# Performance work log

Measured on AMD Instinct MI355X. Metric: run time of the kernel, lower is better.

## Reference

```python
import jax, jax.numpy as jnp
import numpy as np

OFFSET = 1
NUM_ENTITY = 128

def setup_inputs() -> dict:
    key = jax.random.key(0)
    ks = jax.random.split(key, 8)
    B, L, D = 32, 2048, 1024
    M, E, S = 256, NUM_ENTITY, 128
    H, P = 2048, 512
    return {
        "sequence_output": jax.random.normal(ks[0], (B, L, D), dtype=jnp.float32),
        "mention_pos": jax.random.randint(ks[1], (B, M), 0, L - 2),
        "mention2entity": jnp.sort(jax.random.randint(ks[2], (B, M), 0, E), axis=-1),
        "sent_pos": jax.random.randint(ks[3], (B, S), 0, L - 2),
        "fc1_w": jax.random.normal(ks[4], (D, H), dtype=jnp.float32) * 0.02,
        "fc1_b": jnp.zeros((H,), dtype=jnp.float32),
        "fc2_w": jax.random.normal(ks[5], (H, P), dtype=jnp.float32) * 0.02,
        "fc2_b": jnp.zeros((P,), dtype=jnp.float32),
    }

def _segment_logsumexp(x, seg):
    # x: [M, D] mention embeddings, seg: [M] entity ids -> [E, D]
    m = jax.ops.segment_max(x, seg, num_segments=NUM_ENTITY)           # [E, D]
    m_safe = jnp.where(jnp.isfinite(m), m, 0.0)
    s = jax.ops.segment_sum(jnp.exp(x - m_safe[seg]), seg, num_segments=NUM_ENTITY)
    cnt = jax.ops.segment_sum(jnp.ones((x.shape[0],), x.dtype), seg, num_segments=NUM_ENTITY)
    s_safe = jnp.where(cnt[:, None] > 0, s, 1.0)
    lse = jnp.log(s_safe) + m_safe
    # entities with no mentions stay zero (torch.zeros init in original)
    return jnp.where(cnt[:, None] > 0, lse, 0.0)

def reference(sequence_output, mention_pos, mention2entity, sent_pos, fc1_w, fc1_b, fc2_w, fc2_b):
    # gather mention start-token states (offset = +1 as in self.offset)
    mention_embed = jnp.take_along_axis(
        sequence_output, (mention_pos + OFFSET)[:, :, None], axis=1)  # [B, M, D]
    sent_embed = jnp.take_along_axis(
        sequence_output, (sent_pos + OFFSET)[:, :, None], axis=1)     # [B, S, D]
    entity_embed = jax.vmap(_segment_logsumexp)(mention_embed, mention2entity)  # [B, E, D]
    nodes = jnp.concatenate([mention_embed, entity_embed, sent_embed], axis=1)  # [B, M+E+S, D]
    # projection(): fc1 then fc2 (no nonlinearity, as in the original)
    h = jnp.einsum('bnd,dh->bnh', nodes, fc1_w) + fc1_b
    return jnp.einsum('bnh,hp->bnp', h, fc2_w) + fc2_b
```

## Files before the change

### kernel.cpp

```cpp
#include <hip/hip_runtime.h>
#include <cstdint>

#define DEV __device__ __forceinline__

typedef __attribute__((ext_vector_type(8))) short short8;
typedef __attribute__((ext_vector_type(4))) float f32x4;

DEV unsigned short f2bf(float f) {
    uint32_t u = __builtin_bit_cast(uint32_t, f);
    u += 0x7fffu + ((u >> 16) & 1u);
    return (unsigned short)(u >> 16);
}

DEV uint2 pack4(float4 v) {
    uint2 o;
    o.x = (uint32_t)f2bf(v.x) | ((uint32_t)f2bf(v.y) << 16);
    o.y = (uint32_t)f2bf(v.z) | ((uint32_t)f2bf(v.w) << 16);
    return o;
}

DEV void async_copy16(void* lds, const void* g) {
    __builtin_amdgcn_global_load_lds(
        (const __attribute__((address_space(1))) void*)g,
        (__attribute__((address_space(3))) void*)lds, 16, 0, 0);
}

template <int KLEN, int KSTR, int N>
DEV void gemm_body_part(const unsigned short* __restrict__ A,
                        const unsigned short* __restrict__ Bt,
                        float* __restrict__ P,
                        int Mtot, int rowblk, int colblk, int zidx,
                        unsigned short* Al, unsigned short* Bl) {
    int t = threadIdx.x;
    int lane = t & 63, w = t >> 6;
    int wm = w >> 1, wn = w & 1;
    int row0 = rowblk * 128, col0 = colblk * 128;
    size_t kbase = (size_t)zidx * KLEN;
    f32x4 acc[4][4] = {};

    int rifc = lane >> 2;
    int koff = (lane & 3) * 8;
    int c0 = 2 * w, c1 = 2 * w + 1;

    const unsigned short* Abase = A + (size_t)row0 * KSTR + kbase + koff;
    const unsigned short* Bbase = Bt + (size_t)col0 * KSTR + kbase + koff;

    for (int kt = 0; kt < KLEN / 32; ++kt) {
        int k0 = kt * 32;
        __syncthreads();
        async_copy16(&Al[c0 * 512], Abase + (size_t)(c0 * 16 + rifc) * KSTR + k0);
        async_copy16(&Al[c1 * 512], Abase + (size_t)(c1 * 16 + rifc) * KSTR + k0);
        async_copy16(&Bl[c0 * 512], Bbase + (size_t)(c0 * 16 + rifc) * KSTR + k0);
        async_copy16(&Bl[c1 * 512], Bbase + (size_t)(c1 * 16 + rifc) * KSTR + k0);
        __syncthreads();

        int r = lane & 15, kq = lane >> 4;
        short8 a[4], b[4];
        #pragma unroll
        for (int mi = 0; mi < 4; ++mi)
            a[mi] = *reinterpret_cast<const short8*>(&Al[(wm * 64 + mi * 16 + r) * 32 + kq * 8]);
        #pragma unroll
        for (int ni = 0; ni < 4; ++ni)
            b[ni] = *reinterpret_cast<const short8*>(&Bl[(wn * 64 + ni * 16 + r) * 32 + kq * 8]);
        #pragma unroll
        for (int mi = 0; mi < 4; ++mi)
            #pragma unroll
            for (int ni = 0; ni < 4; ++ni)
                acc[mi][ni] = __builtin_amdgcn_mfma_f32_16x16x32_bf16(a[mi], b[ni], acc[mi][ni], 0, 0, 0);
    }

    int r = lane & 15, kq = lane >> 4;
    float* Pz = P + (size_t)zidx * (size_t)N * (size_t)Mtot;
    #pragma unroll
    for (int mi = 0; mi < 4; ++mi)
        #pragma unroll
        for (int ni = 0; ni < 4; ++ni) {
            int col = col0 + wn * 64 + ni * 16 + r;
            #pragma unroll
            for (int j = 0; j < 4; ++j) {
                int row = row0 + wm * 64 + mi * 16 + kq * 4 + j;
                Pz[(size_t)col * Mtot + row] = acc[mi][ni][j];
            }
        }
}

__global__ __launch_bounds__(256) void k_prep(const float* __restrict__ W1,
                                              const float* __restrict__ W2,
                                              const float* __restrict__ b1,
                                              unsigned short* __restrict__ W1c,
                                              unsigned short* __restrict__ W2t,
                                              float* __restrict__ part) {
    __shared__ unsigned short sh[32][33];
    int blk = blockIdx.x, t = threadIdx.x;
    if (blk < 2048) {
        int i = blk * 256 + t;
        float4 v = reinterpret_cast<const float4*>(W1)[i];
        reinterpret_cast<uint2*>(W1c)[i] = pack4(v);
    } else if (blk < 3072) {
        int idx = blk - 2048;
        int h0 = (idx & 63) * 32, p0 = (idx >> 6) * 32;
        int r = t >> 3, c4 = (t & 7) * 4;
        float4 v = *reinterpret_cast<const float4*>(&W2[(size_t)(h0 + r) * 512 + p0 + c4]);
        sh[r][c4 + 0] = f2bf(v.x);
        sh[r][c4 + 1] = f2bf(v.y);
        sh[r][c4 + 2] = f2bf(v.z);
        sh[r][c4 + 3] = f2bf(v.w);
        __syncthreads();
        uint2 o;
        o.x = (uint32_t)sh[c4 + 0][r] | ((uint32_t)sh[c4 + 1][r] << 16);
        o.y = (uint32_t)sh[c4 + 2][r] | ((uint32_t)sh[c4 + 3][r] << 16);
        *reinterpret_cast<uint2*>(&W2t[(size_t)(p0 + r) * 2048 + h0 + c4]) = o;
    } else {
        int hs = blk - 3072;
        float a0 = 0.f, a1 = 0.f;
        #pragma unroll 4
        for (int hh = 0; hh < 32; ++hh) {
            int h = hs * 32 + hh;
            float bb = b1[h];
            a0 += bb * W2[(size_t)h * 512 + t];
            a1 += bb * W2[(size_t)h * 512 + 256 + t];
        }
        part[hs * 512 + t] = a0;
        part[hs * 512 + 256 + t] = a1;
    }
}

__global__ __launch_bounds__(256) void k_mid(const float* __restrict__ seq,
                                             const int* __restrict__ mpos,
                                             const int* __restrict__ m2e,
                                             const unsigned short* __restrict__ W1c,
                                             const unsigned short* __restrict__ W2t,
                                             float* __restrict__ Wpart,
                                             const float* __restrict__ part,
                                             const float* __restrict__ b2,
                                             float* __restrict__ fb,
                                             unsigned short* __restrict__ ent) {
    __shared__ unsigned short Al[128 * 32];
    __shared__ unsigned short Bl[128 * 32];
    __shared__ int sm[256];
    __shared__ int sp[256];
    __shared__ int slo, shi;
    int blk = blockIdx.x, t = threadIdx.x;
    if (blk < 128) {
        gemm_body_part<512, 2048, 512>(W1c, W2t, Wpart, 1024,
                                       (blk >> 2) & 7, blk & 3, blk >> 5, Al, Bl);
    } else if (blk < 130) {
        int p = (blk - 128) * 256 + t;
        float s = b2[p];
        #pragma unroll
        for (int hs = 0; hs < 64; ++hs) s += part[hs * 512 + p];
        fb[p] = s;
    } else {
        int idx = blk - 130;
        int b = idx >> 7, e = idx & 127;
        sm[t] = m2e[b * 256 + t];
        sp[t] = mpos[b * 256 + t] + 1;
        if (t == 0) { slo = 0; shi = 0; }
        __syncthreads();
        if (sm[t] == e && (t == 0 || sm[t - 1] != e)) slo = t;
        if (sm[t] == e && (t == 255 || sm[t + 1] != e)) shi = t + 1;
        __syncthreads();
        int lo = slo, hi = shi;
        float ox, oy, oz, ow;
        if (hi > lo) {
            float s0 = 0.f, s1 = 0.f, s2 = 0.f, s3 = 0.f;
            for (int j = lo; j < hi; ++j) {
                float4 v = *reinterpret_cast<const float4*>(
                    &seq[((size_t)b * 2048 + sp[j]) * 1024 + t * 4]);
                s0 += __expf(v.x); s1 += __expf(v.y);
                s2 += __expf(v.z); s3 += __expf(v.w);
            }
            ox = __logf(s0); oy = __logf(s1);
            oz = __logf(s2); ow = __logf(s3);
        } else {
            ox = oy = oz = ow = 0.f;
        }
        float4 o; o.x = ox; o.y = oy; o.z = oz; o.w = ow;
        *reinterpret_cast<uint2*>(&ent[((size_t)b * 128 + e) * 1024 + t * 4]) = pack4(o);
    }
}

__global__ __launch_bounds__(256) void k_wreduce(const float* __restrict__ P,
                                                 unsigned short* __restrict__ Wt) {
    const size_t SPLIT = 512u * 1024u;
    int i = blockIdx.x * 256 + threadIdx.x;
    float4 a = reinterpret_cast<const float4*>(P)[i];
    float4 b = reinterpret_cast<const float4*>(P + SPLIT)[i];
    float4 c = reinterpret_cast<const float4*>(P + 2 * SPLIT)[i];
    float4 d = reinterpret_cast<const float4*>(P + 3 * SPLIT)[i];
    float4 s;
    s.x = a.x + b.x + c.x + d.x;
    s.y = a.y + b.y + c.y + d.y;
    s.z = a.z + b.z + c.z + d.z;
    s.w = a.w + b.w + c.w + d.w;
    reinterpret_cast<uint2*>(Wt)[i] = pack4(s);
}

__global__ __launch_bounds__(256) void k_gemm_main(const float* __restrict__ seq,
                                                   const int* __restrict__ mpos,
                                                   const int* __restrict__ spos,
                                                   const unsigned short* __restrict__ ent,
                                                   const unsigned short* __restrict__ Wt,
                                                   float* __restrict__ C,
                                                   const float* __restrict__ fb) {
    __shared__ unsigned short Al[128 * 32];
    __shared__ unsigned short Bl[128 * 32];
    int p = blockIdx.x;
    int cpx = gridDim.x >> 3;
    int L = (p & 7) * cpx + (p >> 3);
    int colblk = L & 3;
    int rowblk = L >> 2;

    int t = threadIdx.x;
    int lane = t & 63, w = t >> 6;
    int wm = w >> 1, wn = w & 1;
    int row0 = rowblk * 128, col0 = colblk * 128;
    int b = rowblk >> 2, quad = rowblk & 3;
    f32x4 acc[4][4] = {};

    int rifc = lane >> 2;
    int koff = (lane & 3) * 8;
    int c0 = 2 * w, c1 = 2 * w + 1;
    const unsigned short* Bbase = Wt + (size_t)col0 * 1024 + koff;

    if (quad == 2) {
        const unsigned short* Abase = ent + (size_t)b * 128 * 1024 + koff;
        for (int kt = 0; kt < 32; ++kt) {
            int k0 = kt * 32;
            __syncthreads();
            async_copy16(&Al[c0 * 512], Abase + (size_t)(c0 * 16 + rifc) * 1024 + k0);
            async_copy16(&Al[c1 * 512], Abase + (size_t)(c1 * 16 + rifc) * 1024 + k0);
            async_copy16(&Bl[c0 * 512], Bbase + (size_t)(c0 * 16 + rifc) * 1024 + k0);
            async_copy16(&Bl[c1 * 512], Bbase + (size_t)(c1 * 16 + rifc) * 1024 + k0);
            __syncthreads();
            int r = lane & 15, kq = lane >> 4;
            short8 a[4], bf[4];
            #pragma unroll
            for (int mi = 0; mi < 4; ++mi)
                a[mi] = *reinterpret_cast<const short8*>(&Al[(wm * 64 + mi * 16 + r) * 32 + kq * 8]);
            #pragma unroll
            for (int ni = 0; ni < 4; ++ni)
                bf[ni] = *reinterpret_cast<const short8*>(&Bl[(wn * 64 + ni * 16 + r) * 32 + kq * 8]);
            #pragma unroll
            for (int mi = 0; mi < 4; ++mi)
                #pragma unroll
                for (int ni = 0; ni < 4; ++ni)
                    acc[mi][ni] = __builtin_amdgcn_mfma_f32_16x16x32_bf16(a[mi], bf[ni], acc[mi][ni], 0, 0, 0);
        }
    } else {
        int rloc = t >> 3;
        int cof = (t & 7) * 4;
        const float* rp0; const float* rp1; const float* rp2; const float* rp3;
        {
            int m0, m1, m2, m3;
            if (quad == 3) {
                m0 = spos[b * 128 + rloc] + 1;
                m1 = spos[b * 128 + 32 + rloc] + 1;
                m2 = spos[b * 128 + 64 + rloc] + 1;
                m3 = spos[b * 128 + 96 + rloc] + 1;
            } else {
                int mb = b * 256 + quad * 128;
                m0 = mpos[mb + rloc] + 1;
                m1 = mpos[mb + 32 + rloc] + 1;
                m2 = mpos[mb + 64 + rloc] + 1;
                m3 = mpos[mb + 96 + rloc] + 1;
            }
            rp0 = seq + ((size_t)b * 2048 + m0) * 1024 + cof;
            rp1 = seq + ((size_t)b * 2048 + m1) * 1024 + cof;
            rp2 = seq + ((size_t)b * 2048 + m2) * 1024 + cof;
            rp3 = seq + ((size_t)b * 2048 + m3) * 1024 + cof;
        }
        for (int kt = 0; kt < 32; ++kt) {
            int k0 = kt * 32;
            __syncthreads();
            async_copy16(&Bl[c0 * 512], Bbase + (size_t)(c0 * 16 + rifc) * 1024 + k0);
            async_copy16(&Bl[c1 * 512], Bbase + (size_t)(c1 * 16 + rifc) * 1024 + k0);
            float4 v0 = *reinterpret_cast<const float4*>(rp0 + k0);
            float4 v1 = *reinterpret_cast<const float4*>(rp1 + k0);
            float4 v2 = *reinterpret_cast<const float4*>(rp2 + k0);
            float4 v3 = *reinterpret_cast<const float4*>(rp3 + k0);
            *reinterpret_cast<uint2*>(&Al[(rloc) * 32 + cof])      = pack4(v0);
            *reinterpret_cast<uint2*>(&Al[(32 + rloc) * 32 + cof]) = pack4(v1);
            *reinterpret_cast<uint2*>(&Al[(64 + rloc) * 32 + cof]) = pack4(v2);
            *reinterpret_cast<uint2*>(&Al[(96 + rloc) * 32 + cof]) = pack4(v3);
            __syncthreads();
            int r = lane & 15, kq = lane >> 4;
            short8 a[4], bf[4];
            #pragma unroll
            for (int mi = 0; mi < 4; ++mi)
                a[mi] = *reinterpret_cast<const short8*>(&Al[(wm * 64 + mi * 16 + r) * 32 + kq * 8]);
            #pragma unroll
            for (int ni = 0; ni < 4; ++ni)
                bf[ni] = *reinterpret_cast<const short8*>(&Bl[(wn * 64 + ni * 16 + r) * 32 + kq * 8]);
            #pragma unroll
            for (int mi = 0; mi < 4; ++mi)
                #pragma unroll
                for (int ni = 0; ni < 4; ++ni)
                    acc[mi][ni] = __builtin_amdgcn_mfma_f32_16x16x32_bf16(a[mi], bf[ni], acc[mi][ni], 0, 0, 0);
        }
    }

    int r = lane & 15, kq = lane >> 4;
    #pragma unroll
    for (int mi = 0; mi < 4; ++mi)
        #pragma unroll
        for (int ni = 0; ni < 4; ++ni) {
            int col = col0 + wn * 64 + ni * 16 + r;
            float bv = fb[col];
            #pragma unroll
            for (int j = 0; j < 4; ++j) {
                int row = row0 + wm * 64 + mi * 16 + kq * 4 + j;
                C[(size_t)row * 512 + col] = acc[mi][ni][j] + bv;
            }
        }
}


extern "C" void kernel_launch(void* const* d_in, const int* in_sizes, int n_in,
                              void* d_out, int out_size, void* d_ws, size_t ws_size,
                              hipStream_t stream) {
    const float* seq  = (const float*)d_in[0];
    const int*   mpos = (const int*)d_in[1];
    const int*   m2e  = (const int*)d_in[2];
    const int*   spos = (const int*)d_in[3];
    const float* W1   = (const float*)d_in[4];
    const float* b1   = (const float*)d_in[5];
    const float* W2   = (const float*)d_in[6];
    const float* b2   = (const float*)d_in[7];
    float* out = (float*)d_out;

    char* ws = (char*)d_ws;
    unsigned short* W1c   = (unsigned short*)(ws);
    unsigned short* W2t   = (unsigned short*)(ws + (4u << 20));
    unsigned short* Wt    = (unsigned short*)(ws + (6u << 20));
    float*          Wpart = (float*)(ws + (8u << 20));
    float*          part  = (float*)(ws + (16u << 20));
    float*          fb    = (float*)(ws + (16u << 20) + (1u << 18));
    unsigned short* ent   = (unsigned short*)(ws + (24u << 20));

    k_prep<<<3136, 256, 0, stream>>>(W1, W2, b1, W1c, W2t, part);
    k_mid<<<4226, 256, 0, stream>>>(seq, mpos, m2e, W1c, W2t, Wpart, part, b2, fb, ent);
    k_wreduce<<<512, 256, 0, stream>>>(Wpart, Wt);
    k_gemm_main<<<512, 256, 0, stream>>>(seq, mpos, spos, ent, Wt, out, fb);
}
```

Measured before the change: 66.73 us.

## Fuse weight prep into mid kernel and double-buffer main GEMM

Removes the separate k_prep kernel. The W1·W2 split-K GEMM blocks now load fp32 weights directly, convert them to bf16 in LDS, and transpose W2 on the fly. The fused bias b1·W2 is folded into those blocks and accumulated with atomicAdd into a zeroed fb buffer, and b2 is added in the final GEMM epilogue. The main GEMM also gains double-buffered LDS with prefetch of the next K tile, so loads overlap the MFMA work. The trade-offs are an extra memset launch, atomics, and scattered 2-byte LDS stores for the transposed B tile.

```diff
diff --git a/kernel.cpp b/kernel.cpp
--- a/kernel.cpp
+++ b/kernel.cpp
@@ -25,114 +25,18 @@
         (__attribute__((address_space(3))) void*)lds, 16, 0, 0);
 }
 
-template <int KLEN, int KSTR, int N>
-DEV void gemm_body_part(const unsigned short* __restrict__ A,
-                        const unsigned short* __restrict__ Bt,
-                        float* __restrict__ P,
-                        int Mtot, int rowblk, int colblk, int zidx,
-                        unsigned short* Al, unsigned short* Bl) {
-    int t = threadIdx.x;
-    int lane = t & 63, w = t >> 6;
-    int wm = w >> 1, wn = w & 1;
-    int row0 = rowblk * 128, col0 = colblk * 128;
-    size_t kbase = (size_t)zidx * KLEN;
-    f32x4 acc[4][4] = {};
-
-    int rifc = lane >> 2;
-    int koff = (lane & 3) * 8;
-    int c0 = 2 * w, c1 = 2 * w + 1;
-
-    const unsigned short* Abase = A + (size_t)row0 * KSTR + kbase + koff;
-    const unsigned short* Bbase = Bt + (size_t)col0 * KSTR + kbase + koff;
-
-    for (int kt = 0; kt < KLEN / 32; ++kt) {
-        int k0 = kt * 32;
-        __syncthreads();
-        async_copy16(&Al[c0 * 512], Abase + (size_t)(c0 * 16 + rifc) * KSTR + k0);
-        async_copy16(&Al[c1 * 512], Abase + (size_t)(c1 * 16 + rifc) * KSTR + k0);
-        async_copy16(&Bl[c0 * 512], Bbase + (size_t)(c0 * 16 + rifc) * KSTR + k0);
-        async_copy16(&Bl[c1 * 512], Bbase + (size_t)(c1 * 16 + rifc) * KSTR + k0);
-        __syncthreads();
-
-        int r = lane & 15, kq = lane >> 4;
-        short8 a[4], b[4];
-        #pragma unroll
-        for (int mi = 0; mi < 4; ++mi)
-            a[mi] = *reinterpret_cast<const short8*>(&Al[(wm * 64 + mi * 16 + r) * 32 + kq * 8]);
-        #pragma unroll
-        for (int ni = 0; ni < 4; ++ni)
-            b[ni] = *reinterpret_cast<const short8*>(&Bl[(wn * 64 + ni * 16 + r) * 32 + kq * 8]);
-        #pragma unroll
-        for (int mi = 0; mi < 4; ++mi)
-            #pragma unroll
-            for (int ni = 0; ni < 4; ++ni)
-                acc[mi][ni] = __builtin_amdgcn_mfma_f32_16x16x32_bf16(a[mi], b[ni], acc[mi][ni], 0, 0, 0);
-    }
-
-    int r = lane & 15, kq = lane >> 4;
-    float* Pz = P + (size_t)zidx * (size_t)N * (size_t)Mtot;
-    #pragma unroll
-    for (int mi = 0; mi < 4; ++mi)
-        #pragma unroll
-        for (int ni = 0; ni < 4; ++ni) {
-            int col = col0 + wn * 64 + ni * 16 + r;
-            #pragma unroll
-            for (int j = 0; j < 4; ++j) {
-                int row = row0 + wm * 64 + mi * 16 + kq * 4 + j;
-                Pz[(size_t)col * Mtot + row] = acc[mi][ni][j];
-            }
-        }
-}
-
-__global__ __launch_bounds__(256) void k_prep(const float* __restrict__ W1,
-                                              const float* __restrict__ W2,
-                                              const float* __restrict__ b1,
-                                              unsigned short* __restrict__ W1c,
-                                              unsigned short* __restrict__ W2t,
-                                              float* __restrict__ part) {
-    __shared__ unsigned short sh[32][33];
-    int blk = blockIdx.x, t = threadIdx.x;
-    if (blk < 2048) {
-        int i = blk * 256 + t;
-        float4 v = reinterpret_cast<const float4*>(W1)[i];
-        reinterpret_cast<uint2*>(W1c)[i] = pack4(v);
-    } else if (blk < 3072) {
-        int idx = blk - 2048;
-        int h0 = (idx & 63) * 32, p0 = (idx >> 6) * 32;
-        int r = t >> 3, c4 = (t & 7) * 4;
-        float4 v = *reinterpret_cast<const float4*>(&W2[(size_t)(h0 + r) * 512 + p0 + c4]);
-        sh[r][c4 + 0] = f2bf(v.x);
-        sh[r][c4 + 1] = f2bf(v.y);
-        sh[r][c4 + 2] = f2bf(v.z);
-        sh[r][c4 + 3] = f2bf(v.w);
-        __syncthreads();
-        uint2 o;
-        o.x = (uint32_t)sh[c4 + 0][r] | ((uint32_t)sh[c4 + 1][r] << 16);
-        o.y = (uint32_t)sh[c4 + 2][r] | ((uint32_t)sh[c4 + 3][r] << 16);
-        *reinterpret_cast<uint2*>(&W2t[(size_t)(p0 + r) * 2048 + h0 + c4]) = o;
-    } else {
-        int hs = blk - 3072;
-        float a0 = 0.f, a1 = 0.f;
-        #pragma unroll 4
-        for (int hh = 0; hh < 32; ++hh) {
-            int h = hs * 32 + hh;
-            float bb = b1[h];
-            a0 += bb * W2[(size_t)h * 512 + t];
-            a1 += bb * W2[(size_t)h * 512 + 256 + t];
-        }
-        part[hs * 512 + t] = a0;
-        part[hs * 512 + 256 + t] = a1;
-    }
+DEV float bf2f(unsigned short s) {
+    uint32_t u = (uint32_t)s << 16;
+    return __builtin_bit_cast(float, u);
 }
 
 __global__ __launch_bounds__(256) void k_mid(const float* __restrict__ seq,
                                              const int* __restrict__ mpos,
                                              const int* __restrict__ m2e,
-                                             const unsigned short* __restrict__ W1c,
-                                             const unsigned short* __restrict__ W2t,
+                                             const float* __restrict__ W1,
+                                             const float* __restrict__ W2,
+                                             const float* __restrict__ b1,
                                              float* __restrict__ Wpart,
-                                             const float* __restrict__ part,
-                                             const float* __restrict__ b2,
                                              float* __restrict__ fb,
                                              unsigned short* __restrict__ ent) {
     __shared__ unsigned short Al[128 * 32];
@@ -142,16 +46,80 @@
     __shared__ int slo, shi;
     int blk = blockIdx.x, t = threadIdx.x;
     if (blk < 128) {
-        gemm_body_part<512, 2048, 512>(W1c, W2t, Wpart, 1024,
-                                       (blk >> 2) & 7, blk & 3, blk >> 5, Al, Bl);
-    } else if (blk < 130) {
-        int p = (blk - 128) * 256 + t;
-        float s = b2[p];
-        #pragma unroll
-        for (int hs = 0; hs < 64; ++hs) s += part[hs * 512 + p];
-        fb[p] = s;
+        int rowblk = (blk >> 2) & 7, colblk = blk & 3, z = blk >> 5;
+        int row0 = rowblk * 128, col0 = colblk * 128;
+        int kbase = z * 512;
+        int lane = t & 63, w = t >> 6;
+        int wm = w >> 1, wn = w & 1;
+        f32x4 acc[4][4] = {};
+
+        int rloc = t >> 3, cof = (t & 7) * 4;
+        const float* rpA[4];
+        #pragma unroll
+        for (int j = 0; j < 4; ++j)
+            rpA[j] = W1 + (size_t)(row0 + j * 32 + rloc) * 2048 + kbase + cof;
+        int hh = t >> 5, p4 = (t & 31) * 4;
+        const float* bpB = W2 + (size_t)(kbase + hh) * 512 + col0 + p4;
+
+        bool dofb = (rowblk == 0) && (t < 128);
+        float fbp = 0.f;
+
+        #pragma unroll 1
+        for (int kt = 0; kt < 16; ++kt) {
+            int k0 = kt * 32;
+            __syncthreads();
+            #pragma unroll
+            for (int j = 0; j < 4; ++j) {
+                float4 v = *reinterpret_cast<const float4*>(rpA[j] + k0);
+                *reinterpret_cast<uint2*>(&Al[(j * 32 + rloc) * 32 + cof]) = pack4(v);
+            }
+            #pragma unroll
+            for (int j = 0; j < 4; ++j) {
+                float4 v = *reinterpret_cast<const float4*>(bpB + (size_t)(k0 + 8 * j) * 512);
+                int hl = hh + 8 * j;
+                Bl[(p4 + 0) * 32 + hl] = f2bf(v.x);
+                Bl[(p4 + 1) * 32 + hl] = f2bf(v.y);
+                Bl[(p4 + 2) * 32 + hl] = f2bf(v.z);
+                Bl[(p4 + 3) * 32 + hl] = f2bf(v.w);
+            }
+            __syncthreads();
+            if (dofb) {
+                #pragma unroll 8
+                for (int h = 0; h < 32; ++h)
+                    fbp += b1[kbase + k0 + h] * bf2f(Bl[t * 32 + h]);
+            }
+            int r = lane & 15, kq = lane >> 4;
+            short8 a[4], bfr[4];
+            #pragma unroll
+            for (int mi = 0; mi < 4; ++mi)
+                a[mi] = *reinterpret_cast<const short8*>(&Al[(wm * 64 + mi * 16 + r) * 32 + kq * 8]);
+            #pragma unroll
+            for (int ni = 0; ni < 4; ++ni)
+                bfr[ni] = *reinterpret_cast<const short8*>(&Bl[(wn * 64 + ni * 16 + r) * 32 + kq * 8]);
+            #pragma unroll
+            for (int mi = 0; mi < 4; ++mi)
+                #pragma unroll
+                for (int ni = 0; ni < 4; ++ni)
+                    acc[mi][ni] = __builtin_amdgcn_mfma_f32_16x16x32_bf16(a[mi], bfr[ni], acc[mi][ni], 0, 0, 0);
+        }
+
+        if (dofb) atomicAdd(fb + col0 + t, fbp);
+
+        int r = lane & 15, kq = lane >> 4;
+        float* Pz = Wpart + (size_t)z * 512 * 1024;
+        #pragma unroll
+        for (int mi = 0; mi < 4; ++mi)
+            #pragma unroll
+            for (int ni = 0; ni < 4; ++ni) {
+                int col = col0 + wn * 64 + ni * 16 + r;
+                #pragma unroll
+                for (int j = 0; j < 4; ++j) {
+                    int row = row0 + wm * 64 + mi * 16 + kq * 4 + j;
+                    Pz[(size_t)col * 1024 + row] = acc[mi][ni][j];
+                }
+            }
     } else {
-        int idx = blk - 130;
+        int idx = blk - 128;
         int b = idx >> 7, e = idx & 127;
         sm[t] = m2e[b * 256 + t];
         sp[t] = mpos[b * 256 + t] + 1;
@@ -202,9 +170,10 @@
                                                    const unsigned short* __restrict__ ent,
                                                    const unsigned short* __restrict__ Wt,
                                                    float* __restrict__ C,
-                                                   const float* __restrict__ fb) {
-    __shared__ unsigned short Al[128 * 32];
-    __shared__ unsigned short Bl[128 * 32];
+                                                   const float* __restrict__ fb,
+                                                   const float* __restrict__ b2) {
+    __shared__ unsigned short Al[2][128 * 32];
+    __shared__ unsigned short Bl[2][128 * 32];
     int p = blockIdx.x;
     int cpx = gridDim.x >> 3;
     int L = (p & 7) * cpx + (p >> 3);
@@ -223,34 +192,54 @@
     int c0 = 2 * w, c1 = 2 * w + 1;
     const unsigned short* Bbase = Wt + (size_t)col0 * 1024 + koff;
 
+    auto compute = [&](const unsigned short* AB, const unsigned short* BB) {
+        int r = lane & 15, kq = lane >> 4;
+        short8 a[4], bfr[4];
+        #pragma unroll
+        for (int mi = 0; mi < 4; ++mi)
+            a[mi] = *reinterpret_cast<const short8*>(&AB[(wm * 64 + mi * 16 + r) * 32 + kq * 8]);
+        #pragma unroll
+        for (int ni = 0; ni < 4; ++ni)
+            bfr[ni] = *reinterpret_cast<const short8*>(&BB[(wn * 64 + ni * 16 + r) * 32 + kq * 8]);
+        #pragma unroll
+        for (int mi = 0; mi < 4; ++mi)
+            #pragma unroll
+            for (int ni = 0; ni < 4; ++ni)
+                acc[mi][ni] = __builtin_amdgcn_mfma_f32_16x16x32_bf16(a[mi], bfr[ni], acc[mi][ni], 0, 0, 0);
+    };
+
+    auto stageB = [&](int kt, int buf) {
+        int k0 = kt * 32;
+        async_copy16(&Bl[buf][c0 * 512], Bbase + (size_t)(c0 * 16 + rifc) * 1024 + k0);
+        async_copy16(&Bl[buf][c1 * 512], Bbase + (size_t)(c1 * 16 + rifc) * 1024 + k0);
+    };
+
     if (quad == 2) {
         const unsigned short* Abase = ent + (size_t)b * 128 * 1024 + koff;
-        for (int kt = 0; kt < 32; ++kt) {
+        auto stageA = [&](int kt, int buf) {
             int k0 = kt * 32;
-            __syncthreads();
-            async_copy16(&Al[c0 * 512], Abase + (size_t)(c0 * 16 + rifc) * 1024 + k0);
-            async_copy16(&Al[c1 * 512], Abase + (size_t)(c1 * 16 + rifc) * 1024 + k0);
-            async_copy16(&Bl[c0 * 512], Bbase + (size_t)(c0 * 16 + rifc) * 1024 + k0);
-            async_copy16(&Bl[c1 * 512], Bbase + (size_t)(c1 * 16 + rifc) * 1024 + k0);
-            __syncthreads();
-            int r = lane & 15, kq = lane >> 4;
-            short8 a[4], bf[4];
-            #pragma unroll
-            for (int mi = 0; mi < 4; ++mi)
-                a[mi] = *reinterpret_cast<const short8*>(&Al[(wm * 64 + mi * 16 + r) * 32 + kq * 8]);
-            #pragma unroll
-            for (int ni = 0; ni < 4; ++ni)
-                bf[ni] = *reinterpret_cast<const short8*>(&Bl[(wn * 64 + ni * 16 + r) * 32 + kq * 8]);
-            #pragma unroll
-            for (int mi = 0; mi < 4; ++mi)
-                #pragma unroll
-                for (int ni = 0; ni < 4; ++ni)
-                    acc[mi][ni] = __builtin_amdgcn_mfma_f32_16x16x32_bf16(a[mi], bf[ni], acc[mi][ni], 0, 0, 0);
-        }
+            async_copy16(&Al[buf][c0 * 512], Abase + (size_t)(c0 * 16 + rifc) * 1024 + k0);
+            async_copy16(&Al[buf][c1 * 512], Abase + (size_t)(c1 * 16 + rifc) * 1024 + k0);
+        };
+        stageA(0, 0); stageB(0, 0);
+        __syncthreads();
+        #pragma unroll 1
+        for (int kt = 0; kt < 30; kt += 2) {
+            stageA(kt + 1, 1); stageB(kt + 1, 1);
+            compute(Al[0], Bl[0]);
+            __syncthreads();
+            stageA(kt + 2, 0); stageB(kt + 2, 0);
+            compute(Al[1], Bl[1]);
+            __syncthreads();
+        }
+        stageA(31, 1); stageB(31, 1);
+        compute(Al[0], Bl[0]);
+        __syncthreads();
+        compute(Al[1], Bl[1]);
     } else {
         int rloc = t >> 3;
         int cof = (t & 7) * 4;
-        const float* rp0; const float* rp1; const float* rp2; const float* rp3;
+        const float* rp[4];
         {
             int m0, m1, m2, m3;
             if (quad == 3) {
@@ -265,39 +254,41 @@
                 m2 = mpos[mb + 64 + rloc] + 1;
                 m3 = mpos[mb + 96 + rloc] + 1;
             }
-            rp0 = seq + ((size_t)b * 2048 + m0) * 1024 + cof;
-            rp1 = seq + ((size_t)b * 2048 + m1) * 1024 + cof;
-            rp2 = seq + ((size_t)b * 2048 + m2) * 1024 + cof;
-            rp3 = seq + ((size_t)b * 2048 + m3) * 1024 + cof;
-        }
-        for (int kt = 0; kt < 32; ++kt) {
+            rp[0] = seq + ((size_t)b * 2048 + m0) * 1024 + cof;
+            rp[1] = seq + ((size_t)b * 2048 + m1) * 1024 + cof;
+            rp[2] = seq + ((size_t)b * 2048 + m2) * 1024 + cof;
+            rp[3] = seq + ((size_t)b * 2048 + m3) * 1024 + cof;
+        }
+        float4 va[4];
+        auto loadA = [&](int kt) {
             int k0 = kt * 32;
-            __syncthreads();
-            async_copy16(&Bl[c0 * 512], Bbase + (size_t)(c0 * 16 + rifc) * 1024 + k0);
-            async_copy16(&Bl[c1 * 512], Bbase + (size_t)(c1 * 16 + rifc) * 1024 + k0);
-            float4 v0 = *reinterpret_cast<const float4*>(rp0 + k0);
-            float4 v1 = *reinterpret_cast<const float4*>(rp1 + k0);
-            float4 v2 = *reinterpret_cast<const float4*>(rp2 + k0);
-            float4 v3 = *reinterpret_cast<const float4*>(rp3 + k0);
-            *reinterpret_cast<uint2*>(&Al[(rloc) * 32 + cof])      = pack4(v0);
-            *reinterpret_cast<uint2*>(&Al[(32 + rloc) * 32 + cof]) = pack4(v1);
-            *reinterpret_cast<uint2*>(&Al[(64 + rloc) * 32 + cof]) = pack4(v2);
-            *reinterpret_cast<uint2*>(&Al[(96 + rloc) * 32 + cof]) = pack4(v3);
-            __syncthreads();
-            int r = lane & 15, kq = lane >> 4;
-            short8 a[4], bf[4];
-            #pragma unroll
-            for (int mi = 0; mi < 4; ++mi)
-                a[mi] = *reinterpret_cast<const short8*>(&Al[(wm * 64 + mi * 16 + r) * 32 + kq * 8]);
-            #pragma unroll
-            for (int ni = 0; ni < 4; ++ni)
-                bf[ni] = *reinterpret_cast<const short8*>(&Bl[(wn * 64 + ni * 16 + r) * 32 + kq * 8]);
-            #pragma unroll
-            for (int mi = 0; mi < 4; ++mi)
-                #pragma unroll
-                for (int ni = 0; ni < 4; ++ni)
-                    acc[mi][ni] = __builtin_amdgcn_mfma_f32_16x16x32_bf16(a[mi], bf[ni], acc[mi][ni], 0, 0, 0);
-        }
+            #pragma unroll
+            for (int j = 0; j < 4; ++j)
+                va[j] = *reinterpret_cast<const float4*>(rp[j] + k0);
+        };
+        auto writeA = [&](int buf) {
+            #pragma unroll
+            for (int j = 0; j < 4; ++j)
+                *reinterpret_cast<uint2*>(&Al[buf][(j * 32 + rloc) * 32 + cof]) = pack4(va[j]);
+        };
+        loadA(0); stageB(0, 0); writeA(0);
+        __syncthreads();
+        #pragma unroll 1
+        for (int kt = 0; kt < 30; kt += 2) {
+            loadA(kt + 1); stageB(kt + 1, 1);
+            compute(Al[0], Bl[0]);
+            writeA(1);
+            __syncthreads();
+            loadA(kt + 2); stageB(kt + 2, 0);
+            compute(Al[1], Bl[1]);
+            writeA(0);
+            __syncthreads();
+        }
+        loadA(31); stageB(31, 1);
+        compute(Al[0], Bl[0]);
+        writeA(1);
+        __syncthreads();
+        compute(Al[1], Bl[1]);
     }
 
     int r = lane & 15, kq = lane >> 4;
@@ -306,7 +297,7 @@
         #pragma unroll
         for (int ni = 0; ni < 4; ++ni) {
             int col = col0 + wn * 64 + ni * 16 + r;
-            float bv = fb[col];
+            float bv = fb[col] + b2[col];
             #pragma unroll
             for (int j = 0; j < 4; ++j) {
                 int row = row0 + wm * 64 + mi * 16 + kq * 4 + j;
@@ -330,16 +321,13 @@
     float* out = (float*)d_out;
 
     char* ws = (char*)d_ws;
-    unsigned short* W1c   = (unsigned short*)(ws);
-    unsigned short* W2t   = (unsigned short*)(ws + (4u << 20));
     unsigned short* Wt    = (unsigned short*)(ws + (6u << 20));
     float*          Wpart = (float*)(ws + (8u << 20));
-    float*          part  = (float*)(ws + (16u << 20));
-    float*          fb    = (float*)(ws + (16u << 20) + (1u << 18));
+    float*          fb    = (float*)(ws + (16u << 20));
     unsigned short* ent   = (unsigned short*)(ws + (24u << 20));
 
-    k_prep<<<3136, 256, 0, stream>>>(W1, W2, b1, W1c, W2t, part);
-    k_mid<<<4226, 256, 0, stream>>>(seq, mpos, m2e, W1c, W2t, Wpart, part, b2, fb, ent);
+    hipMemsetAsync((void*)fb, 0, 512 * sizeof(float), stream);
+    k_mid<<<4224, 256, 0, stream>>>(seq, mpos, m2e, W1, W2, b1, Wpart, fb, ent);
     k_wreduce<<<512, 256, 0, stream>>>(Wpart, Wt);
-    k_gemm_main<<<512, 256, 0, stream>>>(seq, mpos, spos, ent, Wt, out, fb);
-}
+    k_gemm_main<<<512, 256, 0, stream>>>(seq, mpos, spos, ent, Wt, out, fb, b2);
+}
```

New measurement: 120.2 us. 1.8x slower.

## Double-buffer LDS in main GEMM and halve column tile to 64

Applied to the files above, without the earlier changes.

The main gathered GEMM now uses two LDS buffers, so the loads for the next k-tile (async B copies, A global loads or async copies) are issued before computing the current tile, with one barrier per step instead of two. The output column tile shrinks from 128 to 64 and the grid doubles to 1024 blocks, giving more parallelism on the many CUs. The cost is that A rows (gathered sequence rows, converted to bf16) are now reloaded for twice as many column blocks, and per-block MFMA work is halved.

```diff
diff --git a/kernel.cpp b/kernel.cpp
--- a/kernel.cpp
+++ b/kernel.cpp
@@ -203,54 +203,73 @@
                                                    const unsigned short* __restrict__ Wt,
                                                    float* __restrict__ C,
                                                    const float* __restrict__ fb) {
-    __shared__ unsigned short Al[128 * 32];
-    __shared__ unsigned short Bl[128 * 32];
+    __shared__ unsigned short Al[2][128 * 32];
+    __shared__ unsigned short Bl[2][64 * 32];
     int p = blockIdx.x;
     int cpx = gridDim.x >> 3;
     int L = (p & 7) * cpx + (p >> 3);
-    int colblk = L & 3;
-    int rowblk = L >> 2;
+    int colblk = L & 7;
+    int rowblk = L >> 3;
 
     int t = threadIdx.x;
     int lane = t & 63, w = t >> 6;
     int wm = w >> 1, wn = w & 1;
-    int row0 = rowblk * 128, col0 = colblk * 128;
+    int row0 = rowblk * 128, col0 = colblk * 64;
     int b = rowblk >> 2, quad = rowblk & 3;
-    f32x4 acc[4][4] = {};
+    f32x4 acc[4][2] = {};
 
     int rifc = lane >> 2;
     int koff = (lane & 3) * 8;
     int c0 = 2 * w, c1 = 2 * w + 1;
-    const unsigned short* Bbase = Wt + (size_t)col0 * 1024 + koff;
+    const unsigned short* BbaseL =
+        Wt + (size_t)(col0 + w * 16 + (lane >> 2)) * 1024 + (lane & 3) * 8;
+
+    auto compute = [&](const unsigned short* AB, const unsigned short* BB) {
+        int r = lane & 15, kq = lane >> 4;
+        short8 a[4], bfr[2];
+        #pragma unroll
+        for (int mi = 0; mi < 4; ++mi)
+            a[mi] = *reinterpret_cast<const short8*>(&AB[(wm * 64 + mi * 16 + r) * 32 + kq * 8]);
+        #pragma unroll
+        for (int ni = 0; ni < 2; ++ni)
+            bfr[ni] = *reinterpret_cast<const short8*>(&BB[(wn * 32 + ni * 16 + r) * 32 + kq * 8]);
+        #pragma unroll
+        for (int mi = 0; mi < 4; ++mi)
+            #pragma unroll
+            for (int ni = 0; ni < 2; ++ni)
+                acc[mi][ni] = __builtin_amdgcn_mfma_f32_16x16x32_bf16(a[mi], bfr[ni], acc[mi][ni], 0, 0, 0);
+    };
+
+    auto stageB = [&](int kt, int buf) {
+        async_copy16(&Bl[buf][w * 16 * 32], BbaseL + kt * 32);
+    };
 
     if (quad == 2) {
         const unsigned short* Abase = ent + (size_t)b * 128 * 1024 + koff;
-        for (int kt = 0; kt < 32; ++kt) {
+        auto stageA = [&](int kt, int buf) {
             int k0 = kt * 32;
+            async_copy16(&Al[buf][c0 * 512], Abase + (size_t)(c0 * 16 + rifc) * 1024 + k0);
+            async_copy16(&Al[buf][c1 * 512], Abase + (size_t)(c1 * 16 + rifc) * 1024 + k0);
+        };
+        stageA(0, 0); stageB(0, 0);
+        __syncthreads();
+        #pragma unroll 1
+        for (int kt = 0; kt < 30; kt += 2) {
+            stageA(kt + 1, 1); stageB(kt + 1, 1);
+            compute(Al[0], Bl[0]);
             __syncthreads();
-            async_copy16(&Al[c0 * 512], Abase + (size_t)(c0 * 16 + rifc) * 1024 + k0);
-            async_copy16(&Al[c1 * 512], Abase + (size_t)(c1 * 16 + rifc) * 1024 + k0);
-            async_copy16(&Bl[c0 * 512], Bbase + (size_t)(c0 * 16 + rifc) * 1024 + k0);
-            async_copy16(&Bl[c1 * 512], Bbase + (size_t)(c1 * 16 + rifc) * 1024 + k0);
+            stageA(kt + 2, 0); stageB(kt + 2, 0);
+            compute(Al[1], Bl[1]);
             __syncthreads();
-            int r = lane & 15, kq = lane >> 4;
-            short8 a[4], bf[4];
-            #pragma unroll
-            for (int mi = 0; mi < 4; ++mi)
-                a[mi] = *reinterpret_cast<const short8*>(&Al[(wm * 64 + mi * 16 + r) * 32 + kq * 8]);
-            #pragma unroll
-            for (int ni = 0; ni < 4; ++ni)
-                bf[ni] = *reinterpret_cast<const short8*>(&Bl[(wn * 64 + ni * 16 + r) * 32 + kq * 8]);
-            #pragma unroll
-            for (int mi = 0; mi < 4; ++mi)
-                #pragma unroll
-                for (int ni = 0; ni < 4; ++ni)
-                    acc[mi][ni] = __builtin_amdgcn_mfma_f32_16x16x32_bf16(a[mi], bf[ni], acc[mi][ni], 0, 0, 0);
-        }
+        }
+        stageA(31, 1); stageB(31, 1);
+        compute(Al[0], Bl[0]);
+        __syncthreads();
+        compute(Al[1], Bl[1]);
     } else {
         int rloc = t >> 3;
         int cof = (t & 7) * 4;
-        const float* rp0; const float* rp1; const float* rp2; const float* rp3;
+        const float* rp[4];
         {
             int m0, m1, m2, m3;
             if (quad == 3) {
@@ -265,47 +284,49 @@
                 m2 = mpos[mb + 64 + rloc] + 1;
                 m3 = mpos[mb + 96 + rloc] + 1;
             }
-            rp0 = seq + ((size_t)b * 2048 + m0) * 1024 + cof;
-            rp1 = seq + ((size_t)b * 2048 + m1) * 1024 + cof;
-            rp2 = seq + ((size_t)b * 2048 + m2) * 1024 + cof;
-            rp3 = seq + ((size_t)b * 2048 + m3) * 1024 + cof;
-        }
-        for (int kt = 0; kt < 32; ++kt) {
+            rp[0] = seq + ((size_t)b * 2048 + m0) * 1024 + cof;
+            rp[1] = seq + ((size_t)b * 2048 + m1) * 1024 + cof;
+            rp[2] = seq + ((size_t)b * 2048 + m2) * 1024 + cof;
+            rp[3] = seq + ((size_t)b * 2048 + m3) * 1024 + cof;
+        }
+        float4 va[4];
+        auto loadA = [&](int kt) {
             int k0 = kt * 32;
+            #pragma unroll
+            for (int j = 0; j < 4; ++j)
+                va[j] = *reinterpret_cast<const float4*>(rp[j] + k0);
+        };
+        auto writeA = [&](int buf) {
+            #pragma unroll
+            for (int j = 0; j < 4; ++j)
+                *reinterpret_cast<uint2*>(&Al[buf][(j * 32 + rloc) * 32 + cof]) = pack4(va[j]);
+        };
+        loadA(0); stageB(0, 0); writeA(0);
+        __syncthreads();
+        #pragma unroll 1
+        for (int kt = 0; kt < 30; kt += 2) {
+            loadA(kt + 1); stageB(kt + 1, 1);
+            compute(Al[0], Bl[0]);
+            writeA(1);
             __syncthreads();
-            async_copy16(&Bl[c0 * 512], Bbase + (size_t)(c0 * 16 + rifc) * 1024 + k0);
-            async_copy16(&Bl[c1 * 512], Bbase + (size_t)(c1 * 16 + rifc) * 1024 + k0);
-            float4 v0 = *reinterpret_cast<const float4*>(rp0 + k0);
-            float4 v1 = *reinterpret_cast<const float4*>(rp1 + k0);
-            float4 v2 = *reinterpret_cast<const float4*>(rp2 + k0);
-            float4 v3 = *reinterpret_cast<const float4*>(rp3 + k0);
-            *reinterpret_cast<uint2*>(&Al[(rloc) * 32 + cof])      = pack4(v0);
-            *reinterpret_cast<uint2*>(&Al[(32 + rloc) * 32 + cof]) = pack4(v1);
-            *reinterpret_cast<uint2*>(&Al[(64 + rloc) * 32 + cof]) = pack4(v2);
-            *reinterpret_cast<uint2*>(&Al[(96 + rloc) * 32 + cof]) = pack4(v3);
+            loadA(kt + 2); stageB(kt + 2, 0);
+            compute(Al[1], Bl[1]);
+            writeA(0);
             __syncthreads();
-            int r = lane & 15, kq = lane >> 4;
-            short8 a[4], bf[4];
-            #pragma unroll
-            for (int mi = 0; mi < 4; ++mi)
-                a[mi] = *reinterpret_cast<const short8*>(&Al[(wm * 64 + mi * 16 + r) * 32 + kq * 8]);
-            #pragma unroll
-            for (int ni = 0; ni < 4; ++ni)
-                bf[ni] = *reinterpret_cast<const short8*>(&Bl[(wn * 64 + ni * 16 + r) * 32 + kq * 8]);
-            #pragma unroll
-            for (int mi = 0; mi < 4; ++mi)
-                #pragma unroll
-                for (int ni = 0; ni < 4; ++ni)
-                    acc[mi][ni] = __builtin_amdgcn_mfma_f32_16x16x32_bf16(a[mi], bf[ni], acc[mi][ni], 0, 0, 0);
-        }
+        }
+        loadA(31); stageB(31, 1);
+        compute(Al[0], Bl[0]);
+        writeA(1);
+        __syncthreads();
+        compute(Al[1], Bl[1]);
     }
 
     int r = lane & 15, kq = lane >> 4;
     #pragma unroll
     for (int mi = 0; mi < 4; ++mi)
         #pragma unroll
-        for (int ni = 0; ni < 4; ++ni) {
-            int col = col0 + wn * 64 + ni * 16 + r;
+        for (int ni = 0; ni < 2; ++ni) {
+            int col = col0 + wn * 32 + ni * 16 + r;
             float bv = fb[col];
             #pragma unroll
             for (int j = 0; j < 4; ++j) {
@@ -341,5 +362,5 @@
     k_prep<<<3136, 256, 0, stream>>>(W1, W2, b1, W1c, W2t, part);
     k_mid<<<4226, 256, 0, stream>>>(seq, mpos, m2e, W1c, W2t, Wpart, part, b2, fb, ent);
     k_wreduce<<<512, 256, 0, stream>>>(Wpart, Wt);
-    k_gemm_main<<<512, 256, 0, stream>>>(seq, mpos, spos, ent, Wt, out, fb);
-}
+    k_gemm_main<<<1024, 256, 0, stream>>>(seq, mpos, spos, ent, Wt, out, fb);
+}
```

Result: slower. 92.96 us (+39.3%).
